# Kernel tuning notes

Measured on AMD Instinct MI355X. Metric: run time of the kernel, lower is better.

The kernel has to match this reference:

```python
import jax, jax.numpy as jnp
import numpy as np


def setup_inputs() -> dict:
    key = jax.random.key(0)
    kq, kk, kv = jax.random.split(key, 3)
    B, L, H, D = 2, 4096, 8, 64
    queries = jax.random.normal(kq, (B, L, H, D), dtype=jnp.float32)
    keys = jax.random.normal(kk, (B, L, H, D), dtype=jnp.float32)
    values = jax.random.normal(kv, (B, L, H, D), dtype=jnp.float32)
    return {"queries": queries, "keys": keys, "values": values}


def reference(queries, keys, values):
    # queries/keys/values: [B, L, H, D]
    d_model = queries.shape[-1]
    scale = 1.0 / jnp.sqrt(jnp.asarray(d_model, dtype=queries.dtype))
    # scores: [B, H, Lq, Lk]
    scores = jnp.einsum('blhd,bshd->bhls', queries, keys)
    # dropout is identity in eval mode / for deterministic reference
    A = jax.nn.softmax(scale * scores, axis=-1)
    # output: [B, Lq, H, D]
    V = jnp.einsum('bhls,bshd->blhd', A, values)
    return V
```

## Files before the change

### kernel.cpp

```cpp
#include <hip/hip_runtime.h>

#define Bn 2
#define Ln 4096
#define Hn 8
#define Dn 64
#define NMEGA 32
#define BH_STRIDE 262144

typedef float    f32x4  __attribute__((ext_vector_type(4)));
typedef float    f32x16 __attribute__((ext_vector_type(16)));
typedef _Float16 f16x2  __attribute__((ext_vector_type(2)));
typedef _Float16 f16x8  __attribute__((ext_vector_type(8)));
typedef unsigned int u32;
typedef u32 u32x2 __attribute__((ext_vector_type(2)));
typedef u32 u32x4 __attribute__((ext_vector_type(4)));

static __device__ __forceinline__ u32 pkf16(float a, float b){
    auto h = __builtin_amdgcn_cvt_pkrtz(a, b);
    return __builtin_bit_cast(u32, h);
}

static __device__ __forceinline__ u32x2 swp(u32 a, u32 b){
    auto r = __builtin_amdgcn_permlane32_swap(a, b, false, false);
    return __builtin_bit_cast(u32x2, r);
}

__global__ __launch_bounds__(256)
void kvprep(const float* __restrict__ Kg, const float* __restrict__ Vg,
            _Float16* __restrict__ kp, _Float16* __restrict__ vp){
    const int t2 = blockIdx.x, bh = blockIdx.y, b = bh>>3, h = bh&7;
    const int tid = threadIdx.x;
    const int w = tid >> 6, lane = tid & 63;
    const int l31 = lane & 31, hi = lane >> 5;
    const int t = t2 >> 1, g = t2 & 1;

    {
        const float* ks = Kg + (((size_t)b*Ln + t2*32 + l31)*Hn + h)*Dn + w*16 + hi*8;
        float4 a  = *(const float4*)ks;
        float4 c4 = *(const float4*)(ks + 4);
        f16x8 o;
        o[0]=(_Float16)a.x;  o[1]=(_Float16)a.y;  o[2]=(_Float16)a.z;  o[3]=(_Float16)a.w;
        o[4]=(_Float16)c4.x; o[5]=(_Float16)c4.y; o[6]=(_Float16)c4.z; o[7]=(_Float16)c4.w;
        *(f16x8*)(kp + (size_t)bh*BH_STRIDE + (size_t)t*4096
                     + (size_t)(g*4 + w)*512 + (size_t)lane*8) = o;
    }

    {
        const int kh = w >> 1, dt = w & 1;
        const float* vs = Vg + (((size_t)b*Ln + t2*32 + kh*16 + hi*8)*Hn + h)*Dn
                        + dt*32 + l31;
        f16x8 o;
#pragma unroll
        for(int j=0;j<8;++j) o[j] = (_Float16)vs[(size_t)j*Hn*Dn];
        *(f16x8*)(vp + (size_t)bh*BH_STRIDE + (size_t)t*4096
                     + (size_t)(g*4 + w)*512 + (size_t)lane*8) = o;
    }
}

static __device__ __forceinline__ f32x16 qk4(const f16x8 (&kf)[4], const f16x8 (&qf)[4]){
    f32x16 s;
#pragma unroll
    for(int r=0;r<16;++r) s[r]=0.f;
    s = __builtin_amdgcn_mfma_f32_32x32x16_f16(kf[0], qf[0], s, 0,0,0);
    s = __builtin_amdgcn_mfma_f32_32x32x16_f16(kf[1], qf[1], s, 0,0,0);
    s = __builtin_amdgcn_mfma_f32_32x32x16_f16(kf[2], qf[2], s, 0,0,0);
    s = __builtin_amdgcn_mfma_f32_32x32x16_f16(kf[3], qf[3], s, 0,0,0);
    return s;
}

static __device__ __forceinline__ void finish_pv(const f32x16& S, float& lac,
                                                 f32x16& o0, f32x16& o1,
                                                 const f16x8 (&vf)[4]){
    f32x16 p;
#pragma unroll
    for(int r=0;r<16;++r) p[r] = __builtin_amdgcn_exp2f(S[r]);
    u32 A0 = pkf16(p[0],p[1]),   A1 = pkf16(p[2],p[3]);
    u32 B0 = pkf16(p[4],p[5]),   B1 = pkf16(p[6],p[7]);
    u32 C0 = pkf16(p[8],p[9]),   C1 = pkf16(p[10],p[11]);
    u32 D0 = pkf16(p[12],p[13]), D1 = pkf16(p[14],p[15]);
    u32x2 r0 = swp(A0,B0), r1 = swp(A1,B1);
    u32x2 r2 = swp(C0,D0), r3 = swp(C1,D1);
    u32x4 w0 = {r0.x, r1.x, r0.y, r1.y};
    u32x4 w1 = {r2.x, r3.x, r2.y, r3.y};
    f16x8 pa0 = __builtin_bit_cast(f16x8, w0);
    f16x8 pa1 = __builtin_bit_cast(f16x8, w1);
    const f16x2 ones = {(_Float16)1.0f, (_Float16)1.0f};
#pragma unroll
    for(int j=0;j<4;++j){
        f16x2 c0 = {pa0[2*j], pa0[2*j+1]};
        f16x2 c1 = {pa1[2*j], pa1[2*j+1]};
        lac = __builtin_amdgcn_fdot2(c0, ones, lac, false);
        lac = __builtin_amdgcn_fdot2(c1, ones, lac, false);
    }
    o0 = __builtin_amdgcn_mfma_f32_32x32x16_f16(pa0, vf[0], o0, 0,0,0);
    o0 = __builtin_amdgcn_mfma_f32_32x32x16_f16(pa1, vf[2], o0, 0,0,0);
    o1 = __builtin_amdgcn_mfma_f32_32x32x16_f16(pa0, vf[1], o1, 0,0,0);
    o1 = __builtin_amdgcn_mfma_f32_32x32x16_f16(pa1, vf[3], o1, 0,0,0);
}

static __device__ __forceinline__ void ld4(f16x8 (&dst)[4], const char* base){
#pragma unroll
    for(int i=0;i<4;++i) dst[i] = *(const f16x8*)(base + (i<<10));
}

__global__ __launch_bounds__(256,2)
void attn_fwd(const float* __restrict__ Qg, float* __restrict__ Og,
              const _Float16* __restrict__ kp, const _Float16* __restrict__ vp){
    __shared__ __align__(16) float xo[8320];

    const int tid  = threadIdx.x;
    const int lane = tid & 63, wv = tid >> 6;
    const int kh2 = wv >> 1, g = wv & 1;
    const int l31 = lane & 31, hi = lane >> 5;
    const int bh = blockIdx.x, b = bh>>3, h = bh&7;
    const int q0 = blockIdx.y*64;

    const float c = 0.125f * 1.4426950408889634f;

    f16x8 qf[2][4];
#pragma unroll
    for(int qt=0;qt<2;++qt){
        const float* qrow = Qg + (((size_t)b*Ln + q0 + qt*32 + l31)*Hn + h)*Dn;
#pragma unroll
        for(int cc=0;cc<4;++cc){
            const float* p4 = qrow + cc*16 + hi*8;
            float4 x = *(const float4*)p4;
            float4 y = *(const float4*)(p4+4);
            f16x8 f;
            f[0]=(_Float16)(x.x*c); f[1]=(_Float16)(x.y*c);
            f[2]=(_Float16)(x.z*c); f[3]=(_Float16)(x.w*c);
            f[4]=(_Float16)(y.x*c); f[5]=(_Float16)(y.y*c);
            f[6]=(_Float16)(y.z*c); f[7]=(_Float16)(y.w*c);
            qf[qt][cc]=f;
        }
    }

    f32x16 o[2][2];
    float lac[2] = {0.f, 0.f};
#pragma unroll
    for(int qt=0;qt<2;++qt)
#pragma unroll
        for(int dt=0;dt<2;++dt)
#pragma unroll
            for(int r=0;r<16;++r) o[qt][dt][r]=0.f;

    const int sub = kh2*8192 + g*4096 + lane*16;
    const char* kgc = (const char*)(kp + (size_t)bh*BH_STRIDE) + sub;
    const char* vgc = (const char*)(vp + (size_t)bh*BH_STRIDE) + sub;

    for(int T=0; T<NMEGA; ++T){
        const char* Kb = kgc + (size_t)T*16384;
        const char* Vb = vgc + (size_t)T*16384;

        f16x8 kf[4], vf[4];
        ld4(kf, Kb); ld4(vf, Vb);

        f32x16 S0 = qk4(kf, qf[0]);
        f32x16 S1 = qk4(kf, qf[1]);
        finish_pv(S0, lac[0], o[0][0], o[0][1], vf);
        finish_pv(S1, lac[1], o[1][0], o[1][1], vf);
    }

    float lred[2];
#pragma unroll
    for(int qt=0;qt<2;++qt)
        lred[qt] = lac[qt] + __shfl_xor(lac[qt], 32, 64);

    float* xb0 = xo;
    float* xb1 = xo + 4096;
    float* xl0 = xo + 8192;
    float* xl1 = xo + 8256;

    if(g==1){
        float* xb = kh2 ? xb1 : xb0;
        float* xl = kh2 ? xl1 : xl0;
#pragma unroll
        for(int qt=0;qt<2;++qt){
#pragma unroll
            for(int dt=0;dt<2;++dt)
#pragma unroll
                for(int r=0;r<16;++r){
                    int qr = (r&3) + 8*(r>>2) + 4*hi;
                    xb[(qt*32 + qr)*64 + dt*32 + l31] = o[qt][dt][r];
                }
            if(hi==0) xl[qt*32 + l31] = lred[qt];
        }
    }
    __syncthreads();
    if(g==0){
        float* xb = kh2 ? xb1 : xb0;
        float* xl = kh2 ? xl1 : xl0;
#pragma unroll
        for(int qt=0;qt<2;++qt){
#pragma unroll
            for(int dt=0;dt<2;++dt)
#pragma unroll
                for(int r=0;r<16;++r){
                    int qr = (r&3) + 8*(r>>2) + 4*hi;
                    o[qt][dt][r] += xb[(qt*32 + qr)*64 + dt*32 + l31];
                }
            lred[qt] += xl[qt*32 + l31];
        }
    }
    __syncthreads();
    if(wv==2){
#pragma unroll
        for(int qt=0;qt<2;++qt){
#pragma unroll
            for(int dt=0;dt<2;++dt)
#pragma unroll
                for(int r=0;r<16;++r){
                    int qr = (r&3) + 8*(r>>2) + 4*hi;
                    xb0[(qt*32 + qr)*64 + dt*32 + l31] = o[qt][dt][r];
                }
            if(hi==0) xl0[qt*32 + l31] = lred[qt];
        }
    }
    __syncthreads();
    if(wv==0){
#pragma unroll
        for(int qt=0;qt<2;++qt){
            float inv = 1.0f/(lred[qt] + xl0[qt*32 + l31]);
            float* ob = Og + (((size_t)b*Ln + q0 + qt*32)*Hn + h)*Dn;
#pragma unroll
            for(int r=0;r<16;++r){
                int qr = (r&3) + 8*(r>>2) + 4*hi;
                float invr = __shfl(inv, qr, 64);
                float v0 = o[qt][0][r] + xb0[(qt*32 + qr)*64 +  0 + l31];
                float v1 = o[qt][1][r] + xb0[(qt*32 + qr)*64 + 32 + l31];
                ob[(size_t)qr*Hn*Dn +  0 + l31] = v0*invr;
                ob[(size_t)qr*Hn*Dn + 32 + l31] = v1*invr;
            }
        }
    }
}

extern "C" void kernel_launch(void* const* d_in, const int* in_sizes, int n_in,
                              void* d_out, int out_size, void* d_ws, size_t ws_size,
                              hipStream_t stream) {
    const float* Q = (const float*)d_in[0];
    const float* K = (const float*)d_in[1];
    const float* V = (const float*)d_in[2];
    float* O = (float*)d_out;

    _Float16* kp = (_Float16*)d_ws;
    _Float16* vp = (_Float16*)((char*)d_ws + (8u<<20));

    kvprep<<<dim3(128, 16), dim3(256), 0, stream>>>(K, V, kp, vp);
    attn_fwd<<<dim3(16, 64), dim3(256), 0, stream>>>(Q, O, kp, vp);
}
```

Baseline: 168.5 us.

## Stage K/V tiles through LDS with async global-to-LDS prefetch of next tile

Replaces the per-wave direct global loads of the packed fp16 K/V tiles with block-wide global_load_lds transfers into a shared buffer. The buffer is reused from the epilogue scratch. The next tile is issued right after the current one is read into registers, so its transfer can overlap the QK and PV MFMA work. This aims to hide global memory latency in the main loop, at the cost of two block barriers per iteration and a single-buffered LDS round trip with no data reuse across waves.

Result: slower. 178.1 us (+5.7%).

```diff
diff --git a/kernel.cpp b/kernel.cpp
--- a/kernel.cpp
+++ b/kernel.cpp
@@ -14,6 +14,12 @@
 typedef unsigned int u32;
 typedef u32 u32x2 __attribute__((ext_vector_type(2)));
 typedef u32 u32x4 __attribute__((ext_vector_type(4)));
+
+static __device__ __forceinline__ void gld16(const void* g, void* l){
+    __builtin_amdgcn_global_load_lds(
+        (const __attribute__((address_space(1))) unsigned int*)g,
+        (__attribute__((address_space(3))) unsigned int*)l, 16, 0, 0);
+}
 
 static __device__ __forceinline__ u32 pkf16(float a, float b){
     auto h = __builtin_amdgcn_cvt_pkrtz(a, b);
@@ -98,15 +104,11 @@
     o1 = __builtin_amdgcn_mfma_f32_32x32x16_f16(pa1, vf[3], o1, 0,0,0);
 }
 
-static __device__ __forceinline__ void ld4(f16x8 (&dst)[4], const char* base){
-#pragma unroll
-    for(int i=0;i<4;++i) dst[i] = *(const f16x8*)(base + (i<<10));
-}
-
 __global__ __launch_bounds__(256,2)
 void attn_fwd(const float* __restrict__ Qg, float* __restrict__ Og,
               const _Float16* __restrict__ kp, const _Float16* __restrict__ vp){
-    __shared__ __align__(16) float xo[8320];
+    __shared__ __align__(16) float xo[8448];
+    _Float16* sKV = (_Float16*)xo;
 
     const int tid  = threadIdx.x;
     const int lane = tid & 63, wv = tid >> 6;
@@ -144,17 +146,38 @@
 #pragma unroll
             for(int r=0;r<16;++r) o[qt][dt][r]=0.f;
 
-    const int sub = kh2*8192 + g*4096 + lane*16;
-    const char* kgc = (const char*)(kp + (size_t)bh*BH_STRIDE) + sub;
-    const char* vgc = (const char*)(vp + (size_t)bh*BH_STRIDE) + sub;
+    const _Float16* kg = kp + (size_t)bh*BH_STRIDE;
+    const _Float16* vg = vp + (size_t)bh*BH_STRIDE;
+
+    const char* sKb = (const char*)sKV + kh2*8192 + g*4096 + lane*16;
+    const char* sVb = sKb + 16384;
+
+#pragma unroll
+    for(int i=0;i<4;++i){
+        int u = i*256 + tid;
+        gld16(kg + (size_t)u*8, sKV + (size_t)u*8);
+        gld16(vg + (size_t)u*8, sKV + 8192 + (size_t)u*8);
+    }
 
     for(int T=0; T<NMEGA; ++T){
-        const char* Kb = kgc + (size_t)T*16384;
-        const char* Vb = vgc + (size_t)T*16384;
-
+        __syncthreads();
         f16x8 kf[4], vf[4];
-        ld4(kf, Kb); ld4(vf, Vb);
-
+#pragma unroll
+        for(int i=0;i<4;++i){
+            kf[i] = *(const f16x8*)(sKb + (i<<10));
+            vf[i] = *(const f16x8*)(sVb + (i<<10));
+        }
+        __syncthreads();
+        if(T+1 < NMEGA){
+            const _Float16* kgn = kg + (size_t)(T+1)*8192;
+            const _Float16* vgn = vg + (size_t)(T+1)*8192;
+#pragma unroll
+            for(int i=0;i<4;++i){
+                int u = i*256 + tid;
+                gld16(kgn + (size_t)u*8, sKV + (size_t)u*8);
+                gld16(vgn + (size_t)u*8, sKV + 8192 + (size_t)u*8);
+            }
+        }
         f32x16 S0 = qk4(kf, qf[0]);
         f32x16 S1 = qk4(kf, qf[1]);
         finish_pv(S0, lac[0], o[0][0], o[0][1], vf);
@@ -166,6 +189,7 @@
     for(int qt=0;qt<2;++qt)
         lred[qt] = lac[qt] + __shfl_xor(lac[qt], 32, 64);
 
+    __syncthreads();
     float* xb0 = xo;
     float* xb1 = xo + 4096;
     float* xl0 = xo + 8192;
```
